# Kernel tuning notes

Measured on AMD Instinct MI355X. Metric: run time of the kernel, lower is better.

Reference implementation:

```python
import jax, jax.numpy as jnp
import numpy as np

E, D, O, G, H, K = 8, 1024, 1024, 512, 2048, 2
B = 8192

def _xavier(key, shape):
    fan_in, fan_out = shape[-2], shape[-1]
    lim = float(np.sqrt(6.0 / (fan_in + fan_out)))
    return jax.random.uniform(key, shape, jnp.float32, -lim, lim)

def setup_inputs() -> dict:
    key = jax.random.key(0)
    ks = jax.random.split(key, 6)
    x = jax.random.normal(ks[0], (B, D), jnp.float32)
    # stacked expert params (xavier-uniform weights, zero bias like torch init)
    W1 = _xavier(ks[1], (E, D, H))
    b1 = jnp.zeros((E, H), jnp.float32)
    W2 = _xavier(ks[2], (E, H, O))
    b2 = jnp.zeros((E, O), jnp.float32)
    # gate params
    Wg1 = _xavier(ks[3], (D, G))
    bg1 = jnp.zeros((G,), jnp.float32)
    Wg2 = _xavier(ks[4], (G, E))
    bg2 = jnp.zeros((E,), jnp.float32)
    return {"x": x, "W1": W1, "b1": b1, "W2": W2, "b2": b2,
            "Wg1": Wg1, "bg1": bg1, "Wg2": Wg2, "bg2": bg2}

def reference(x, W1, b1, W2, b2, Wg1, bg1, Wg2, bg2):
    batch = x.shape[0]
    # gate (dropout inactive in eval)
    gate_logits = jax.nn.relu(x @ Wg1 + bg1) @ Wg2 + bg2          # [B,E]
    gate_scores = jax.nn.softmax(gate_logits, axis=1)
    top_k_scores, top_k_indices = jax.lax.top_k(gate_scores, K)   # [B,K]
    # dense all-expert MLP (mirrors torch.stack over experts)
    h = jax.nn.relu(jnp.einsum('bd,edh->ebh', x, W1) + b1[:, None, :])   # [E,B,H]
    expert_outputs = jnp.einsum('ebh,eho->beo', h, W2) + b2[None, :, :]  # [B,E,O]
    # gather top-k expert outputs, scale, combine
    selected = jnp.take_along_axis(expert_outputs, top_k_indices[:, :, None], axis=1)  # [B,K,O]
    scaled = selected * top_k_scores[:, :, None]
    scaled = scaled / (jnp.sum(top_k_scores, axis=1, keepdims=True)[:, :, None] + 1e-9)
    combined = jnp.sum(scaled, axis=1)                            # [B,O]
    # auxiliary loss
    one_hot = jax.nn.one_hot(top_k_indices, E, dtype=jnp.float32) # [B,K,E]
    expert_load = jnp.sum(one_hot, axis=(0, 1)) / (batch + 1e-9)
    load_balancing_loss = jnp.var(expert_load, ddof=1)            # torch var is unbiased
    entropy = -jnp.mean(jnp.sum(gate_scores * jnp.log(gate_scores + 1e-9), axis=1))
    aux_loss = load_balancing_loss + entropy
    return combined, aux_loss
```

## Files before the change

kernel.cpp:

```cpp
#include <hip/hip_runtime.h>

#define B_ 8192
#define D_ 1024
#define O_ 1024
#define G_ 512
#define H_ 2048
#define E_ 8
#define ROWSP (B_ * 2 + E_ * 128)
#define TAU 0.01f

typedef unsigned short u16;
using f32x4 = __attribute__((ext_vector_type(4))) float;
using s16x8 = __attribute__((ext_vector_type(8))) short;

__device__ __forceinline__ u16 f2bf(float f) {
  union { float f; unsigned u; } v; v.f = f;
  unsigned r = v.u + 0x7FFFu + ((v.u >> 16) & 1u);
  return (u16)(r >> 16);
}
__device__ __forceinline__ float bf2f(u16 h) {
  union { unsigned u; float f; } v; v.u = ((unsigned)h) << 16; return v.f;
}
__device__ __forceinline__ void gload16(const void* g, void* l) {
  __builtin_amdgcn_global_load_lds(
      (const __attribute__((address_space(1))) unsigned int*)g,
      (__attribute__((address_space(3))) unsigned int*)l, 16, 0, 0);
}

__global__ __launch_bounds__(256) void k_cast_x(const float* __restrict__ x,
                                                u16* __restrict__ xhi,
                                                u16* __restrict__ xlo) {
  int t = blockIdx.x * 256 + threadIdx.x;
  float4 v = ((const float4*)x)[t];
  u16 h0 = f2bf(v.x), h1 = f2bf(v.y), h2 = f2bf(v.z), h3 = f2bf(v.w);
  ushort4 hi; hi.x = h0; hi.y = h1; hi.z = h2; hi.w = h3;
  ushort4 lo;
  lo.x = f2bf(v.x - bf2f(h0)); lo.y = f2bf(v.y - bf2f(h1));
  lo.z = f2bf(v.z - bf2f(h2)); lo.w = f2bf(v.w - bf2f(h3));
  ((ushort4*)xhi)[t] = hi; ((ushort4*)xlo)[t] = lo;
}

__global__ __launch_bounds__(256) void k_transpose_cast(const float* __restrict__ src,
                                                        u16* __restrict__ dhi,
                                                        u16* __restrict__ dlo,
                                                        int R, int C) {
  __shared__ float tile[32][33];
  size_t bofs = (size_t)blockIdx.z * R * C;
  src += bofs; dhi += bofs; if (dlo) dlo += bofs;
  int tx = threadIdx.x & 31, ty = threadIdx.x >> 5;
  int c0 = blockIdx.x * 32, r0 = blockIdx.y * 32;
#pragma unroll
  for (int p = 0; p < 4; ++p) {
    int r = ty + p * 8;
    tile[r][tx] = src[(size_t)(r0 + r) * C + c0 + tx];
  }
  __syncthreads();
#pragma unroll
  for (int p = 0; p < 4; ++p) {
    int r = ty + p * 8;
    float v = tile[tx][r];
    size_t o = (size_t)(c0 + r) * R + r0 + tx;
    dhi[o] = f2bf(v);
    if (dlo) dlo[o] = f2bf(v - bf2f(f2bf(v)));
  }
}

__global__ __launch_bounds__(256) void k_gate_gemm1(const u16* __restrict__ xhi,
                                                    const u16* __restrict__ xlo,
                                                    const u16* __restrict__ whi,
                                                    const u16* __restrict__ wlo,
                                                    const float* __restrict__ bg1,
                                                    float* __restrict__ G1) {
  __shared__ u16 Ah[128 * 32], Al[128 * 32], Bh[128 * 32], Bl[128 * 32];
  int t = threadIdx.x;
  int wave = t >> 6, lane = t & 63;
  int wm = wave >> 1, wn = wave & 1;
  int m0 = blockIdx.y * 128, n0 = blockIdx.x * 128;

  const f32x4 z = {0.f, 0.f, 0.f, 0.f};
  f32x4 acc[4][4];
#pragma unroll
  for (int i = 0; i < 4; ++i)
#pragma unroll
    for (int j = 0; j < 4; ++j) acc[i][j] = z;

  int ac = (t & 3) * 8;
  for (int k0 = 0; k0 < D_; k0 += 32) {
#pragma unroll
    for (int r = 0; r < 2; ++r) {
      int li = r * 256 + t;
      int row = li >> 2;
      gload16(xhi + (size_t)(m0 + row) * D_ + k0 + ac, &Ah[li * 8]);
      gload16(xlo + (size_t)(m0 + row) * D_ + k0 + ac, &Al[li * 8]);
      gload16(whi + (size_t)(n0 + row) * D_ + k0 + ac, &Bh[li * 8]);
      gload16(wlo + (size_t)(n0 + row) * D_ + k0 + ac, &Bl[li * 8]);
    }
    __syncthreads();
    s16x8 ah[4], al[4], bh[4], bl[4];
#pragma unroll
    for (int i = 0; i < 4; ++i) {
      int ra = (wm * 64 + i * 16 + (lane & 15)) * 32 + (lane >> 4) * 8;
      int rb = (wn * 64 + i * 16 + (lane & 15)) * 32 + (lane >> 4) * 8;
      ah[i] = *(const s16x8*)&Ah[ra]; al[i] = *(const s16x8*)&Al[ra];
      bh[i] = *(const s16x8*)&Bh[rb]; bl[i] = *(const s16x8*)&Bl[rb];
    }
#pragma unroll
    for (int i = 0; i < 4; ++i)
#pragma unroll
      for (int j = 0; j < 4; ++j) {
        acc[i][j] = __builtin_amdgcn_mfma_f32_16x16x32_bf16(ah[i], bh[j], acc[i][j], 0, 0, 0);
        acc[i][j] = __builtin_amdgcn_mfma_f32_16x16x32_bf16(ah[i], bl[j], acc[i][j], 0, 0, 0);
        acc[i][j] = __builtin_amdgcn_mfma_f32_16x16x32_bf16(al[i], bh[j], acc[i][j], 0, 0, 0);
      }
    __syncthreads();
  }
#pragma unroll
  for (int j = 0; j < 4; ++j) {
    int col = n0 + wn * 64 + j * 16 + (lane & 15);
    float bias = bg1[col];
#pragma unroll
    for (int i = 0; i < 4; ++i)
#pragma unroll
      for (int q = 0; q < 4; ++q) {
        int row = m0 + wm * 64 + i * 16 + (lane >> 4) * 4 + q;
        float v = acc[i][j][q] + bias;
        G1[(size_t)row * G_ + col] = v > 0.f ? v : 0.f;
      }
  }
}

__global__ __launch_bounds__(256) void k_gate_logits(const float* __restrict__ G1,
                                                     const float* __restrict__ Wg2,
                                                     const float* __restrict__ bg2,
                                                     float* __restrict__ logits,
                                                     int* __restrict__ flaglist,
                                                     int* __restrict__ nflag) {
  int t = threadIdx.x, wave = t >> 6, lane = t & 63;
  int row = blockIdx.x * 4 + wave;

  float4 g0 = *(const float4*)(G1 + (size_t)row * G_ + lane * 8);
  float4 g1 = *(const float4*)(G1 + (size_t)row * G_ + lane * 8 + 4);
  float g[8] = {g0.x, g0.y, g0.z, g0.w, g1.x, g1.y, g1.z, g1.w};
  float p[8] = {0, 0, 0, 0, 0, 0, 0, 0};
#pragma unroll
  for (int cc = 0; cc < 8; ++cc) {
    int c = lane * 8 + cc;
    float4 w0 = *(const float4*)(Wg2 + c * 8);
    float4 w1 = *(const float4*)(Wg2 + c * 8 + 4);
    p[0] += g[cc] * w0.x; p[1] += g[cc] * w0.y; p[2] += g[cc] * w0.z; p[3] += g[cc] * w0.w;
    p[4] += g[cc] * w1.x; p[5] += g[cc] * w1.y; p[6] += g[cc] * w1.z; p[7] += g[cc] * w1.w;
  }
#pragma unroll
  for (int off = 32; off >= 1; off >>= 1)
#pragma unroll
    for (int e = 0; e < 8; ++e) p[e] += __shfl_xor(p[e], off);
  if (lane == 0) {
    float l1 = -1e30f, l2 = -1e30f, l3 = -1e30f;
#pragma unroll
    for (int e = 0; e < 8; ++e) {
      float v = p[e] + bg2[e];
      logits[(size_t)row * 8 + e] = v;
      if (v > l1) { l3 = l2; l2 = l1; l1 = v; }
      else if (v > l2) { l3 = l2; l2 = v; }
      else if (v > l3) { l3 = v; }
    }
    if (l2 - l3 < TAU) {
      int pos = atomicAdd(nflag, 1);
      flaglist[pos] = row;
    }
  }
}

__global__ __launch_bounds__(256) void k_gate_fixup(const float* __restrict__ x,
                                                    const float* __restrict__ Wg1,
                                                    const float* __restrict__ bg1,
                                                    const float* __restrict__ Wg2,
                                                    const float* __restrict__ bg2,
                                                    const int* __restrict__ flaglist,
                                                    const int* __restrict__ nflag,
                                                    float* __restrict__ logits) {
  __shared__ float xs[1024];
  __shared__ float red[256][9];
  int t = threadIdx.x;
  int n = *nflag;
  for (int i = blockIdx.x; i < n; i += gridDim.x) {
    int row = flaglist[i];
    ((float4*)xs)[t] = ((const float4*)(x + (size_t)row * D_))[t];
    __syncthreads();
    int c0 = t * 2;
    float h0 = 0.f, h1 = 0.f;
#pragma unroll 8
    for (int d = 0; d < D_; ++d) {
      float xv = xs[d];
      float2 w = *(const float2*)(Wg1 + (size_t)d * G_ + c0);
      h0 += xv * w.x; h1 += xv * w.y;
    }
    h0 += bg1[c0]; h1 += bg1[c0 + 1];
    h0 = h0 > 0.f ? h0 : 0.f; h1 = h1 > 0.f ? h1 : 0.f;
#pragma unroll
    for (int e = 0; e < 8; ++e)
      red[t][e] = h0 * Wg2[c0 * 8 + e] + h1 * Wg2[(c0 + 1) * 8 + e];
    __syncthreads();
    for (int s = 128; s >= 1; s >>= 1) {
      if (t < s) {
#pragma unroll
        for (int e = 0; e < 8; ++e) red[t][e] += red[t + s][e];
      }
      __syncthreads();
    }
    if (t < 8) logits[(size_t)row * 8 + t] = red[0][t] + bg2[t];
    __syncthreads();
  }
}

__global__ __launch_bounds__(256) void k_gate_final(const float* __restrict__ logits,
                                                    int* __restrict__ topidx,
                                                    float* __restrict__ wnorm,
                                                    int* __restrict__ counts,
                                                    float* __restrict__ entacc) {
  __shared__ int cnt_s[8];
  __shared__ float ent_s[4];
  int t = threadIdx.x;
  if (t < 8) cnt_s[t] = 0;
  __syncthreads();
  int row = blockIdx.x * 256 + t;
  float4 a = ((const float4*)logits)[(size_t)row * 2];
  float4 b = ((const float4*)logits)[(size_t)row * 2 + 1];
  float L[8] = {a.x, a.y, a.z, a.w, b.x, b.y, b.z, b.w};
  float m = L[0];
#pragma unroll
  for (int e = 1; e < 8; ++e) m = fmaxf(m, L[e]);
  float s[8], Z = 0.f;
#pragma unroll
  for (int e = 0; e < 8; ++e) { s[e] = expf(L[e] - m); Z += s[e]; }
  float inv = 1.f / Z;
  float sc[8];
#pragma unroll
  for (int e = 0; e < 8; ++e) sc[e] = s[e] * inv;
  int i1 = 0;
#pragma unroll
  for (int e = 1; e < 8; ++e) if (L[e] > L[i1]) i1 = e;
  int i2 = (i1 == 0) ? 1 : 0;
#pragma unroll
  for (int e = 0; e < 8; ++e) if (e != i1 && L[e] > L[i2]) i2 = e;
  float s1 = sc[i1], s2 = sc[i2];
  float denom = s1 + s2 + 1e-9f;
  topidx[row * 2] = i1; topidx[row * 2 + 1] = i2;
  wnorm[row * 2] = s1 / denom; wnorm[row * 2 + 1] = s2 / denom;
  atomicAdd(&cnt_s[i1], 1); atomicAdd(&cnt_s[i2], 1);
  float ent = 0.f;
#pragma unroll
  for (int e = 0; e < 8; ++e) ent -= sc[e] * logf(sc[e] + 1e-9f);
#pragma unroll
  for (int off = 32; off >= 1; off >>= 1) ent += __shfl_xor(ent, off);
  if ((t & 63) == 0) ent_s[t >> 6] = ent;
  __syncthreads();
  if (t == 0) atomicAdd(entacc, ent_s[0] + ent_s[1] + ent_s[2] + ent_s[3]);
  if (t < 8) atomicAdd(&counts[t], cnt_s[t]);
}

__global__ void k_scan(const int* __restrict__ counts, const float* __restrict__ entacc,
                       int* __restrict__ aoff, float* __restrict__ aux_out) {
  if (threadIdx.x == 0 && blockIdx.x == 0) {
    int off = 0; aoff[0] = 0;
    float ld[8]; float mean = 0.f;
    for (int e = 0; e < 8; ++e) {
      ld[e] = (float)counts[e] / (8192.0f + 1e-9f);
      mean += ld[e];
      off += ((counts[e] + 127) >> 7) << 7;
      aoff[e + 1] = off;
    }
    mean *= 0.125f;
    float var = 0.f;
    for (int e = 0; e < 8; ++e) { float d = ld[e] - mean; var += d * d; }
    var *= (1.0f / 7.0f);
    *aux_out = var + entacc[0] / 8192.0f;
  }
}

__global__ __launch_bounds__(256) void k_scatter(const int* __restrict__ topidx,
                                                 const float* __restrict__ wnorm,
                                                 const int* __restrict__ aoff,
                                                 int* __restrict__ fill,
                                                 int* __restrict__ tok_list,
                                                 float* __restrict__ wroute) {
  int t = blockIdx.x * 256 + threadIdx.x;
  if (t >= B_ * 2) return;
  int e = topidx[t];
  int pos = aoff[e] + atomicAdd(&fill[e], 1);
  tok_list[pos] = t >> 1;
  wroute[pos] = wnorm[t];
}

__global__ __launch_bounds__(256) void k_egemm1(const u16* __restrict__ xhi,
                                                const u16* __restrict__ w1t,
                                                const float* __restrict__ b1v,
                                                const int* __restrict__ tok_list,
                                                const int* __restrict__ aoff,
                                                u16* __restrict__ hbuf) {
  __shared__ u16 As[128 * 32], Bs[128 * 32];
  int rt = blockIdx.y;
  int row0 = rt * 128;
  if (row0 >= aoff[8]) return;
  int e = 0;
  while (row0 >= aoff[e + 1]) ++e;
  int n0 = blockIdx.x * 128;
  int t = threadIdx.x, wave = t >> 6, lane = t & 63;
  int wm = wave >> 1, wn = wave & 1;
  const u16* w1e = w1t + (size_t)e * H_ * D_;

  int arow = t >> 2, ac = (t & 3) * 8;
  int tok0 = tok_list[row0 + arow];       if (tok0 < 0) tok0 = 0;
  int tok1 = tok_list[row0 + 64 + arow];  if (tok1 < 0) tok1 = 0;
  const u16* a0 = xhi + (size_t)tok0 * D_ + ac;
  const u16* a1 = xhi + (size_t)tok1 * D_ + ac;
  const u16* bb0 = w1e + (size_t)(n0 + arow) * D_ + ac;
  const u16* bb1 = w1e + (size_t)(n0 + 64 + arow) * D_ + ac;

  const f32x4 z = {0.f, 0.f, 0.f, 0.f};
  f32x4 acc[4][4];
#pragma unroll
  for (int i = 0; i < 4; ++i)
#pragma unroll
    for (int j = 0; j < 4; ++j) acc[i][j] = z;

  for (int k0 = 0; k0 < D_; k0 += 32) {
    gload16(a0 + k0, &As[t * 8]);
    gload16(a1 + k0, &As[(256 + t) * 8]);
    gload16(bb0 + k0, &Bs[t * 8]);
    gload16(bb1 + k0, &Bs[(256 + t) * 8]);
    __syncthreads();
    s16x8 af[4], bf[4];
#pragma unroll
    for (int i = 0; i < 4; ++i) {
      af[i] = *(const s16x8*)&As[(wm * 64 + i * 16 + (lane & 15)) * 32 + (lane >> 4) * 8];
      bf[i] = *(const s16x8*)&Bs[(wn * 64 + i * 16 + (lane & 15)) * 32 + (lane >> 4) * 8];
    }
#pragma unroll
    for (int i = 0; i < 4; ++i)
#pragma unroll
      for (int j = 0; j < 4; ++j)
        acc[i][j] = __builtin_amdgcn_mfma_f32_16x16x32_bf16(af[i], bf[j], acc[i][j], 0, 0, 0);
    __syncthreads();
  }
#pragma unroll
  for (int j = 0; j < 4; ++j) {
    int col = n0 + wn * 64 + j * 16 + (lane & 15);
    float bias = b1v[e * H_ + col];
#pragma unroll
    for (int i = 0; i < 4; ++i)
#pragma unroll
      for (int q = 0; q < 4; ++q) {
        int row = row0 + wm * 64 + i * 16 + (lane >> 4) * 4 + q;
        float v = acc[i][j][q] + bias;
        hbuf[(size_t)row * H_ + col] = f2bf(v > 0.f ? v : 0.f);
      }
  }
}

__global__ __launch_bounds__(256) void k_egemm2(const u16* __restrict__ hbuf,
                                                const u16* __restrict__ w2t,
                                                const float* __restrict__ b2v,
                                                const int* __restrict__ tok_list,
                                                const int* __restrict__ aoff,
                                                const float* __restrict__ wroute,
                                                float* __restrict__ out) {
  __shared__ u16 As[128 * 32], Bs[128 * 32];
  int rt = blockIdx.y;
  int row0 = rt * 128;
  if (row0 >= aoff[8]) return;
  int e = 0;
  while (row0 >= aoff[e + 1]) ++e;
  int n0 = blockIdx.x * 128;
  int t = threadIdx.x, wave = t >> 6, lane = t & 63;
  int wm = wave >> 1, wn = wave & 1;
  const u16* w2e = w2t + (size_t)e * O_ * H_;

  int arow = t >> 2, ac = (t & 3) * 8;
  const u16* a0 = hbuf + (size_t)(row0 + arow) * H_ + ac;
  const u16* a1 = hbuf + (size_t)(row0 + 64 + arow) * H_ + ac;
  const u16* bb0 = w2e + (size_t)(n0 + arow) * H_ + ac;
  const u16* bb1 = w2e + (size_t)(n0 + 64 + arow) * H_ + ac;

  const f32x4 z = {0.f, 0.f, 0.f, 0.f};
  f32x4 acc[4][4];
#pragma unroll
  for (int i = 0; i < 4; ++i)
#pragma unroll
    for (int j = 0; j < 4; ++j) acc[i][j] = z;

  for (int k0 = 0; k0 < H_; k0 += 32) {
    gload16(a0 + k0, &As[t * 8]);
    gload16(a1 + k0, &As[(256 + t) * 8]);
    gload16(bb0 + k0, &Bs[t * 8]);
    gload16(bb1 + k0, &Bs[(256 + t) * 8]);
    __syncthreads();
    s16x8 af[4], bf[4];
#pragma unroll
    for (int i = 0; i < 4; ++i) {
      af[i] = *(const s16x8*)&As[(wm * 64 + i * 16 + (lane & 15)) * 32 + (lane >> 4) * 8];
      bf[i] = *(const s16x8*)&Bs[(wn * 64 + i * 16 + (lane & 15)) * 32 + (lane >> 4) * 8];
    }
#pragma unroll
    for (int i = 0; i < 4; ++i)
#pragma unroll
      for (int j = 0; j < 4; ++j)
        acc[i][j] = __builtin_amdgcn_mfma_f32_16x16x32_bf16(af[i], bf[j], acc[i][j], 0, 0, 0);
    __syncthreads();
  }
#pragma unroll
  for (int j = 0; j < 4; ++j) {
    int col = n0 + wn * 64 + j * 16 + (lane & 15);
    float bias = b2v[e * O_ + col];
#pragma unroll
    for (int i = 0; i < 4; ++i)
#pragma unroll
      for (int q = 0; q < 4; ++q) {
        int pr = row0 + wm * 64 + i * 16 + (lane >> 4) * 4 + q;
        int tk = tok_list[pr];
        if (tk >= 0) {
          float wv = wroute[pr];
          atomicAdd(&out[(size_t)tk * O_ + col], (acc[i][j][q] + bias) * wv);
        }
      }
  }
}

static const size_t o_xhi  = 0;
static const size_t o_xlo  = o_xhi + (size_t)B_ * D_ * 2;
static const size_t o_w1t  = o_xlo + (size_t)B_ * D_ * 2;
static const size_t o_w2t  = o_w1t + (size_t)E_ * H_ * D_ * 2;
static const size_t o_wg1h = o_w2t + (size_t)E_ * O_ * H_ * 2;
static const size_t o_wg1l = o_wg1h + (size_t)G_ * D_ * 2;
static const size_t o_G1   = o_wg1l + (size_t)G_ * D_ * 2;
static const size_t o_h    = o_G1 + (size_t)B_ * G_ * 4;
static const size_t o_idx  = o_h + (size_t)ROWSP * H_ * 2;
static const size_t o_wn   = o_idx + (size_t)B_ * 2 * 4;
static const size_t o_tok  = o_wn + (size_t)B_ * 2 * 4;
static const size_t o_wr   = o_tok + (size_t)ROWSP * 4;
static const size_t o_cnt  = o_wr + (size_t)ROWSP * 4;
static const size_t o_fill = o_cnt + 32;
static const size_t o_ent  = o_cnt + 64;
static const size_t o_nfl  = o_cnt + 96;
static const size_t o_aoff = o_cnt + 128;
static const size_t o_logits = o_cnt + 256;
static const size_t o_flag   = o_logits + (size_t)B_ * 8 * 4;

extern "C" void kernel_launch(void* const* d_in, const int* in_sizes, int n_in,
                              void* d_out, int out_size, void* d_ws, size_t ws_size,
                              hipStream_t stream) {
  const float* x   = (const float*)d_in[0];
  const float* W1  = (const float*)d_in[1];
  const float* b1  = (const float*)d_in[2];
  const float* W2  = (const float*)d_in[3];
  const float* b2  = (const float*)d_in[4];
  const float* Wg1 = (const float*)d_in[5];
  const float* bg1 = (const float*)d_in[6];
  const float* Wg2 = (const float*)d_in[7];
  const float* bg2 = (const float*)d_in[8];
  float* out = (float*)d_out;
  char* ws = (char*)d_ws;

  u16* xhi  = (u16*)(ws + o_xhi);
  u16* xlo  = (u16*)(ws + o_xlo);
  u16* w1t  = (u16*)(ws + o_w1t);
  u16* w2t  = (u16*)(ws + o_w2t);
  u16* wg1h = (u16*)(ws + o_wg1h);
  u16* wg1l = (u16*)(ws + o_wg1l);
  float* G1 = (float*)(ws + o_G1);
  u16* hbuf = (u16*)(ws + o_h);
  int* topidx = (int*)(ws + o_idx);
  float* wnorm = (float*)(ws + o_wn);
  int* tok_list = (int*)(ws + o_tok);
  float* wroute = (float*)(ws + o_wr);
  int* counts = (int*)(ws + o_cnt);
  int* fill = (int*)(ws + o_fill);
  float* entacc = (float*)(ws + o_ent);
  int* nflag = (int*)(ws + o_nfl);
  int* aoff = (int*)(ws + o_aoff);
  float* logits = (float*)(ws + o_logits);
  int* flaglist = (int*)(ws + o_flag);

  hipMemsetAsync(out, 0, (size_t)out_size * 4, stream);
  hipMemsetAsync(ws + o_cnt, 0, 128, stream);
  hipMemsetAsync(ws + o_tok, 0xFF, (size_t)ROWSP * 4, stream);

  k_cast_x<<<(B_ * D_ / 4) / 256, 256, 0, stream>>>(x, xhi, xlo);
  k_transpose_cast<<<dim3(G_ / 32, D_ / 32, 1), 256, 0, stream>>>(Wg1, wg1h, wg1l, D_, G_);
  k_transpose_cast<<<dim3(H_ / 32, D_ / 32, E_), 256, 0, stream>>>(W1, w1t, nullptr, D_, H_);
  k_transpose_cast<<<dim3(O_ / 32, H_ / 32, E_), 256, 0, stream>>>(W2, w2t, nullptr, H_, O_);

  k_gate_gemm1<<<dim3(G_ / 128, B_ / 128), 256, 0, stream>>>(xhi, xlo, wg1h, wg1l, bg1, G1);
  k_gate_logits<<<B_ / 4, 256, 0, stream>>>(G1, Wg2, bg2, logits, flaglist, nflag);
  k_gate_fixup<<<128, 256, 0, stream>>>(x, Wg1, bg1, Wg2, bg2, flaglist, nflag, logits);
  k_gate_final<<<B_ / 256, 256, 0, stream>>>(logits, topidx, wnorm, counts, entacc);
  k_scan<<<1, 64, 0, stream>>>(counts, entacc, aoff, out + (size_t)B_ * O_);
  k_scatter<<<(B_ * 2) / 256, 256, 0, stream>>>(topidx, wnorm, aoff, fill, tok_list, wroute);

  k_egemm1<<<dim3(H_ / 128, ROWSP / 128), 256, 0, stream>>>(xhi, w1t, b1, tok_list, aoff, hbuf);
  k_egemm2<<<dim3(O_ / 128, ROWSP / 128), 256, 0, stream>>>(hbuf, w2t, b2, tok_list, aoff, wroute, out);
}
```

Baseline: 574.1 us.

## Replace atomic scatter-add with bf16 routed buffer, combine kernel, and XCD swizzle

The second expert GEMM now writes weighted outputs as bf16 into a row-per-routed-slot buffer instead of doing fp32 atomicAdd into the output. A new combine kernel sums the two slots per token using a position map recorded by the scatter kernel. This removes the output memset, the tok_list memset and the atomic traffic. Separately, the GEMM grids are flattened and remapped so neighbouring tiles land on the same XCD for better L2 reuse. The trade-off is an extra kernel, an extra buffer round-trip, and bf16 rounding of partial outputs; padding rows in tok_list are no longer initialised, so they are clamped by a range check.

```diff
diff --git a/kernel.cpp b/kernel.cpp
--- a/kernel.cpp
+++ b/kernel.cpp
@@ -25,6 +25,9 @@
   __builtin_amdgcn_global_load_lds(
       (const __attribute__((address_space(1))) unsigned int*)g,
       (__attribute__((address_space(3))) unsigned int*)l, 16, 0, 0);
+}
+__device__ __forceinline__ int xcd_swz(int bid, int nwg) {
+  return (bid & 7) * (nwg >> 3) + (bid >> 3);
 }
 
 __global__ __launch_bounds__(256) void k_cast_x(const float* __restrict__ x,
@@ -72,10 +75,11 @@
                                                     const float* __restrict__ bg1,
                                                     float* __restrict__ G1) {
   __shared__ u16 Ah[128 * 32], Al[128 * 32], Bh[128 * 32], Bl[128 * 32];
+  int work = xcd_swz(blockIdx.x, (G_ / 128) * (B_ / 128));
+  int m0 = (work >> 2) * 128, n0 = (work & 3) * 128;
   int t = threadIdx.x;
   int wave = t >> 6, lane = t & 63;
   int wm = wave >> 1, wn = wave & 1;
-  int m0 = blockIdx.y * 128, n0 = blockIdx.x * 128;
 
   const f32x4 z = {0.f, 0.f, 0.f, 0.f};
   f32x4 acc[4][4];
@@ -283,13 +287,15 @@
                                                  const int* __restrict__ aoff,
                                                  int* __restrict__ fill,
                                                  int* __restrict__ tok_list,
-                                                 float* __restrict__ wroute) {
+                                                 float* __restrict__ wroute,
+                                                 int* __restrict__ pos_of) {
   int t = blockIdx.x * 256 + threadIdx.x;
   if (t >= B_ * 2) return;
   int e = topidx[t];
   int pos = aoff[e] + atomicAdd(&fill[e], 1);
   tok_list[pos] = t >> 1;
   wroute[pos] = wnorm[t];
+  pos_of[t] = pos;
 }
 
 __global__ __launch_bounds__(256) void k_egemm1(const u16* __restrict__ xhi,
@@ -299,19 +305,20 @@
                                                 const int* __restrict__ aoff,
                                                 u16* __restrict__ hbuf) {
   __shared__ u16 As[128 * 32], Bs[128 * 32];
-  int rt = blockIdx.y;
+  int work = xcd_swz(blockIdx.x, (H_ / 128) * (ROWSP / 128));
+  int rt = work >> 4;
+  int n0 = (work & 15) * 128;
   int row0 = rt * 128;
   if (row0 >= aoff[8]) return;
   int e = 0;
   while (row0 >= aoff[e + 1]) ++e;
-  int n0 = blockIdx.x * 128;
   int t = threadIdx.x, wave = t >> 6, lane = t & 63;
   int wm = wave >> 1, wn = wave & 1;
   const u16* w1e = w1t + (size_t)e * H_ * D_;
 
   int arow = t >> 2, ac = (t & 3) * 8;
-  int tok0 = tok_list[row0 + arow];       if (tok0 < 0) tok0 = 0;
-  int tok1 = tok_list[row0 + 64 + arow];  if (tok1 < 0) tok1 = 0;
+  int tok0 = tok_list[row0 + arow];       if ((unsigned)tok0 >= B_) tok0 = 0;
+  int tok1 = tok_list[row0 + 64 + arow];  if ((unsigned)tok1 >= B_) tok1 = 0;
   const u16* a0 = xhi + (size_t)tok0 * D_ + ac;
   const u16* a1 = xhi + (size_t)tok1 * D_ + ac;
   const u16* bb0 = w1e + (size_t)(n0 + arow) * D_ + ac;
@@ -361,17 +368,17 @@
 __global__ __launch_bounds__(256) void k_egemm2(const u16* __restrict__ hbuf,
                                                 const u16* __restrict__ w2t,
                                                 const float* __restrict__ b2v,
-                                                const int* __restrict__ tok_list,
                                                 const int* __restrict__ aoff,
                                                 const float* __restrict__ wroute,
-                                                float* __restrict__ out) {
+                                                u16* __restrict__ rbuf) {
   __shared__ u16 As[128 * 32], Bs[128 * 32];
-  int rt = blockIdx.y;
+  int work = xcd_swz(blockIdx.x, (O_ / 128) * (ROWSP / 128));
+  int rt = work >> 3;
+  int n0 = (work & 7) * 128;
   int row0 = rt * 128;
   if (row0 >= aoff[8]) return;
   int e = 0;
   while (row0 >= aoff[e + 1]) ++e;
-  int n0 = blockIdx.x * 128;
   int t = threadIdx.x, wave = t >> 6, lane = t & 63;
   int wm = wave >> 1, wn = wave & 1;
   const u16* w2e = w2t + (size_t)e * O_ * H_;
@@ -409,21 +416,38 @@
     __syncthreads();
   }
 #pragma unroll
-  for (int j = 0; j < 4; ++j) {
-    int col = n0 + wn * 64 + j * 16 + (lane & 15);
-    float bias = b2v[e * O_ + col];
-#pragma unroll
-    for (int i = 0; i < 4; ++i)
-#pragma unroll
-      for (int q = 0; q < 4; ++q) {
-        int pr = row0 + wm * 64 + i * 16 + (lane >> 4) * 4 + q;
-        int tk = tok_list[pr];
-        if (tk >= 0) {
-          float wv = wroute[pr];
-          atomicAdd(&out[(size_t)tk * O_ + col], (acc[i][j][q] + bias) * wv);
-        }
+  for (int i = 0; i < 4; ++i)
+#pragma unroll
+    for (int q = 0; q < 4; ++q) {
+      int row = row0 + wm * 64 + i * 16 + (lane >> 4) * 4 + q;
+      float wv = wroute[row];
+#pragma unroll
+      for (int j = 0; j < 4; ++j) {
+        int col = n0 + wn * 64 + j * 16 + (lane & 15);
+        float bias = b2v[e * O_ + col];
+        rbuf[(size_t)row * O_ + col] = f2bf((acc[i][j][q] + bias) * wv);
       }
-  }
+    }
+}
+
+__global__ __launch_bounds__(256) void k_combine(const u16* __restrict__ rbuf,
+                                                 const int* __restrict__ pos_of,
+                                                 float* __restrict__ out) {
+  int t = threadIdx.x;
+  int tok = blockIdx.x * 2 + (t >> 7);
+  int c = (t & 127) * 8;
+  int p0 = pos_of[tok * 2], p1 = pos_of[tok * 2 + 1];
+  const u16* r0 = rbuf + (size_t)p0 * O_ + c;
+  const u16* r1 = rbuf + (size_t)p1 * O_ + c;
+  ushort4 a0 = *(const ushort4*)r0, a1 = *(const ushort4*)(r0 + 4);
+  ushort4 b0 = *(const ushort4*)r1, b1 = *(const ushort4*)(r1 + 4);
+  float4 o0, o1;
+  o0.x = bf2f(a0.x) + bf2f(b0.x); o0.y = bf2f(a0.y) + bf2f(b0.y);
+  o0.z = bf2f(a0.z) + bf2f(b0.z); o0.w = bf2f(a0.w) + bf2f(b0.w);
+  o1.x = bf2f(a1.x) + bf2f(b1.x); o1.y = bf2f(a1.y) + bf2f(b1.y);
+  o1.z = bf2f(a1.z) + bf2f(b1.z); o1.w = bf2f(a1.w) + bf2f(b1.w);
+  float* op = out + (size_t)tok * O_ + c;
+  *(float4*)op = o0; *(float4*)(op + 4) = o1;
 }
 
 static const size_t o_xhi  = 0;
@@ -436,7 +460,8 @@
 static const size_t o_h    = o_G1 + (size_t)B_ * G_ * 4;
 static const size_t o_idx  = o_h + (size_t)ROWSP * H_ * 2;
 static const size_t o_wn   = o_idx + (size_t)B_ * 2 * 4;
-static const size_t o_tok  = o_wn + (size_t)B_ * 2 * 4;
+static const size_t o_pos  = o_wn + (size_t)B_ * 2 * 4;
+static const size_t o_tok  = o_pos + (size_t)B_ * 2 * 4;
 static const size_t o_wr   = o_tok + (size_t)ROWSP * 4;
 static const size_t o_cnt  = o_wr + (size_t)ROWSP * 4;
 static const size_t o_fill = o_cnt + 32;
@@ -445,6 +470,7 @@
 static const size_t o_aoff = o_cnt + 128;
 static const size_t o_logits = o_cnt + 256;
 static const size_t o_flag   = o_logits + (size_t)B_ * 8 * 4;
+static const size_t o_rbuf = o_xlo;
 
 extern "C" void kernel_launch(void* const* d_in, const int* in_sizes, int n_in,
                               void* d_out, int out_size, void* d_ws, size_t ws_size,
@@ -471,6 +497,7 @@
   u16* hbuf = (u16*)(ws + o_h);
   int* topidx = (int*)(ws + o_idx);
   float* wnorm = (float*)(ws + o_wn);
+  int* pos_of = (int*)(ws + o_pos);
   int* tok_list = (int*)(ws + o_tok);
   float* wroute = (float*)(ws + o_wr);
   int* counts = (int*)(ws + o_cnt);
@@ -480,23 +507,23 @@
   int* aoff = (int*)(ws + o_aoff);
   float* logits = (float*)(ws + o_logits);
   int* flaglist = (int*)(ws + o_flag);
-
-  hipMemsetAsync(out, 0, (size_t)out_size * 4, stream);
+  u16* rbuf = (u16*)(ws + o_rbuf);
+
   hipMemsetAsync(ws + o_cnt, 0, 128, stream);
-  hipMemsetAsync(ws + o_tok, 0xFF, (size_t)ROWSP * 4, stream);
 
   k_cast_x<<<(B_ * D_ / 4) / 256, 256, 0, stream>>>(x, xhi, xlo);
   k_transpose_cast<<<dim3(G_ / 32, D_ / 32, 1), 256, 0, stream>>>(Wg1, wg1h, wg1l, D_, G_);
   k_transpose_cast<<<dim3(H_ / 32, D_ / 32, E_), 256, 0, stream>>>(W1, w1t, nullptr, D_, H_);
   k_transpose_cast<<<dim3(O_ / 32, H_ / 32, E_), 256, 0, stream>>>(W2, w2t, nullptr, H_, O_);
 
-  k_gate_gemm1<<<dim3(G_ / 128, B_ / 128), 256, 0, stream>>>(xhi, xlo, wg1h, wg1l, bg1, G1);
+  k_gate_gemm1<<<(G_ / 128) * (B_ / 128), 256, 0, stream>>>(xhi, xlo, wg1h, wg1l, bg1, G1);
   k_gate_logits<<<B_ / 4, 256, 0, stream>>>(G1, Wg2, bg2, logits, flaglist, nflag);
   k_gate_fixup<<<128, 256, 0, stream>>>(x, Wg1, bg1, Wg2, bg2, flaglist, nflag, logits);
   k_gate_final<<<B_ / 256, 256, 0, stream>>>(logits, topidx, wnorm, counts, entacc);
   k_scan<<<1, 64, 0, stream>>>(counts, entacc, aoff, out + (size_t)B_ * O_);
-  k_scatter<<<(B_ * 2) / 256, 256, 0, stream>>>(topidx, wnorm, aoff, fill, tok_list, wroute);
-
-  k_egemm1<<<dim3(H_ / 128, ROWSP / 128), 256, 0, stream>>>(xhi, w1t, b1, tok_list, aoff, hbuf);
-  k_egemm2<<<dim3(O_ / 128, ROWSP / 128), 256, 0, stream>>>(hbuf, w2t, b2, tok_list, aoff, wroute, out);
-}
+  k_scatter<<<(B_ * 2) / 256, 256, 0, stream>>>(topidx, wnorm, aoff, fill, tok_list, wroute, pos_of);
+
+  k_egemm1<<<(H_ / 128) * (ROWSP / 128), 256, 0, stream>>>(xhi, w1t, b1, tok_list, aoff, hbuf);
+  k_egemm2<<<(O_ / 128) * (ROWSP / 128), 256, 0, stream>>>(hbuf, w2t, b2, aoff, wroute, rbuf);
+  k_combine<<<B_ / 2, 256, 0, stream>>>(rbuf, pos_of, out);
+}
```

Result: faster. 526.2 us (-8.3%).
